# Performance work log

Measured on AMD Instinct MI355X. Metric: run time of the kernel, lower is better.

## Reference

```python
import jax, jax.numpy as jnp
import numpy as np

EMB_SIZE = 200000
DIM = 256
WALK_LEN = 80
WINDOW = 5
BATCH = 32
NEGATIVE = 5
NEG_WEIGHT = 1.0
LR = 0.025
LAP_NORM = 0.01


def _pos_index():
    # replicates init_emb2pos_index: for each center i, u-index = context j, v-index = center i
    us, vs = [], []
    for i in range(WALK_LEN):
        for j in range(max(0, i - WINDOW), i):
            us.append(j); vs.append(i)
        for j in range(i + 1, min(WALK_LEN, i + 1 + WINDOW)):
            us.append(j); vs.append(i)
    us = np.asarray(us, np.int32)
    vs = np.asarray(vs, np.int32)
    off = (np.arange(BATCH, dtype=np.int32) * WALK_LEN)[:, None]
    return (us[None, :] + off).reshape(-1), (vs[None, :] + off).reshape(-1)


def _neg_index(pos_v):
    # replicates init_emb2neg_index: u-index = center repeated NEGATIVE times per positive pair;
    # v-index = shuffled node positions from the whole batch (in-batch negatives)
    negu = np.repeat(pos_v, NEGATIVE)
    negv = np.tile(np.arange(BATCH * WALK_LEN, dtype=np.int32), NEGATIVE * WINDOW * 2)
    rng = np.random.default_rng(0)
    rng.shuffle(negv)
    return negu, negv[: len(negu)]


def setup_inputs() -> dict:
    key = jax.random.key(0)
    k1, k2, k3 = jax.random.split(key, 3)
    initrange = 1.0 / DIM
    u_weight = jax.random.uniform(k1, (EMB_SIZE, DIM), jnp.float32, -initrange, initrange)
    # original inits v to zero; use small noise so scores/grads are non-degenerate for testing
    v_weight = 0.01 * jax.random.normal(k2, (EMB_SIZE, DIM), jnp.float32)
    # sigmoid lookup table: torch.sigmoid(torch.arange(-6.01, 6.01, 0.01)) -> 1202 entries
    table = jax.nn.sigmoid(jnp.arange(1202, dtype=jnp.float32) * 0.01 - 6.01)
    table = table.at[0].set(0.0).at[-1].set(1.0)
    nodes = jax.random.randint(k3, (BATCH, WALK_LEN), 0, EMB_SIZE, dtype=jnp.int32)
    pu, pv = _pos_index()
    nu, nv = _neg_index(pv)
    return {
        "nodes": nodes,
        "u_weight": u_weight,
        "v_weight": v_weight,
        "lookup_table": table,
        "idx_posu": jnp.asarray(pu),
        "idx_posv": jnp.asarray(pv),
        "idx_negu": jnp.asarray(nu),
        "idx_negv": jnp.asarray(nv),
    }


def reference(nodes, u_weight, v_weight, lookup_table, idx_posu, idx_posv, idx_negu, idx_negv):
    flat = nodes.reshape(-1)                       # [B*L]
    emb_u = u_weight[flat]                         # [B*L, D]
    emb_v = v_weight[flat]                         # [B*L, D]

    def fast_sigmoid(s):
        idx = jnp.floor((s + 6.01) / 0.01).astype(jnp.int32)
        return lookup_table[idx]

    # positive pairs
    epu = emb_u[idx_posu]                          # [P, D]
    epv = emb_v[idx_posv]
    pos = jnp.clip(jnp.sum(epu * epv, axis=1), -6.0, 6.0)
    s = (1.0 - fast_sigmoid(pos))[:, None]
    gu_pos = s * epv + LAP_NORM * (epv - epu)
    gv_pos = s * epu + LAP_NORM * (epu - epv)
    grad_u = jnp.zeros_like(emb_u).at[idx_posu].add(gu_pos)
    grad_v = jnp.zeros_like(emb_v).at[idx_posv].add(gv_pos)

    # in-batch negative pairs
    enu = emb_u[idx_negu]                          # [P*neg, D]
    env = emb_v[idx_negv]
    neg = jnp.clip(jnp.sum(enu * env, axis=1), -6.0, 6.0)
    ns = (-fast_sigmoid(neg))[:, None]
    grad_u = grad_u.at[idx_negu].add(NEG_WEIGHT * ns * env)
    grad_v = grad_v.at[idx_negv].add(NEG_WEIGHT * ns * enu)

    # fused SGD scatter-update of the embedding tables
    new_u = u_weight.at[flat].add(LR * grad_u)
    new_v = v_weight.at[flat].add(LR * grad_v)
    return jnp.concatenate([new_u, new_v], axis=0)  # [2*EMB_SIZE, D]
```

## Files before the change

### kernel.cpp

```cpp
#include <hip/hip_runtime.h>

#define EMB      200000
#define DIM      256
#define WALK     80
#define WIN      5
#define BATCH    32
#define PPW      770
#define NPOSN    (BATCH * PPW)
#define NNEG     (NPOSN * 5)
#define NPOSIT   (BATCH * WALK)
#define LR       0.025f
#define LAP      0.01f
#define INV_STRIDE 64

#define T4          (EMB * DIM / 4)
#define CHUNK_F4    2048
#define COPY_CHUNKS (2 * T4 / CHUNK_F4)

#define INV_BLOCKS  482
#define OWN_BLOCKS  10
#define GRAD_BLOCKS 1280

typedef __attribute__((ext_vector_type(4))) int v4i;
typedef __attribute__((ext_vector_type(4))) float v4f;

__device__ __forceinline__ int Sfun(int i) {
    if (i <= 5)  return 5 * i + (i * (i - 1)) / 2;
    if (i <= 75) return 35 + 10 * (i - 5);
    return 735 + (i - 75) * 84 - ((i + 74) * (i - 75)) / 2;
}

__device__ __forceinline__ float wave_sum(float s) {
#pragma unroll
    for (int off = 32; off > 0; off >>= 1) s += __shfl_xor(s, off, 64);
    return s;
}

__device__ __forceinline__ float fast_sig(const float* __restrict__ t, float d) {
    float s = fminf(fmaxf(d, -6.0f), 6.0f);
    int idx = (int)floorf((s + 6.01f) / 0.01f);
    return t[idx];
}

__global__ void __launch_bounds__(256) k_stage(
        const int* __restrict__ nodes,
        const float* __restrict__ uw,
        const float* __restrict__ vw,
        float* __restrict__ eu,
        float* __restrict__ ev,
        v4f* __restrict__ accz,
        v4i* __restrict__ markz,
        int* __restrict__ cnt) {
    int p = blockIdx.x;
    int d = threadIdx.x;
    int node = nodes[p];
    eu[p * DIM + d] = uw[(size_t)node * DIM + d];
    ev[p * DIM + d] = vw[(size_t)node * DIM + d];
    int tid = p * 256 + d;
    if (tid < (2 * NPOSIT * DIM) / 4) accz[tid] = (v4f){0.f, 0.f, 0.f, 0.f};
    if (tid < EMB / 4) markz[tid] = (v4i){0x7FFFFFFF, 0x7FFFFFFF, 0x7FFFFFFF, 0x7FFFFFFF};
    if (d == 0) cnt[p] = 0;
}

__global__ void k_index(const int* __restrict__ negv,
                        const int* __restrict__ nodes,
                        int* __restrict__ cnt,
                        int* __restrict__ inv,
                        int* __restrict__ mark) {
    int bid = blockIdx.x;
    if (bid < INV_BLOCKS) {
        int m = bid * 256 + threadIdx.x;
        if (m < NNEG) {
            int p = negv[m];
            int slot = atomicAdd(&cnt[p], 1);
            inv[p * INV_STRIDE + slot] = m;
        }
    } else {
        int p = (bid - INV_BLOCKS) * 256 + threadIdx.x;
        if (p < NPOSIT) atomicMin(&mark[nodes[p]], p);
    }
}

__global__ void __launch_bounds__(256) k_grad(
        const int*   __restrict__ nodes,
        const float* __restrict__ table,
        const int*   __restrict__ negu,
        const int*   __restrict__ negv,
        const float* __restrict__ eu,
        const float* __restrict__ ev,
        const int*   __restrict__ cnt,
        const int*   __restrict__ inv,
        const int*   __restrict__ mark,
        float*       __restrict__ accu,
        float*       __restrict__ accv) {
    int wid  = blockIdx.x * 4 + (threadIdx.x >> 6);
    int lane = threadIdx.x & 63;
    int side = wid >= NPOSIT;
    int p    = side ? wid - NPOSIT : wid;
    int b    = p / WALK;
    int i    = p - b * WALK;
    int col  = lane * 4;

    int jlo = (i - WIN < 0) ? 0 : i - WIN;
    int jhi = (i + WIN > WALK - 1) ? WALK - 1 : i + WIN;
    int own = mark[nodes[p]];

    if (!side) {
        const float4 mu = *(const float4*)&eu[p * DIM + col];
        float gx = 0.f, gy = 0.f, gz = 0.f, gw = 0.f;

        for (int j = jlo; j <= jhi; ++j) {
            if (j == i) continue;
            int q = b * WALK + j;
            float4 qv = *(const float4*)&ev[q * DIM + col];
            float d1 = wave_sum(mu.x * qv.x + mu.y * qv.y + mu.z * qv.z + mu.w * qv.w);
            float s1 = 1.0f - fast_sig(table, d1);
            gx += s1 * qv.x + LAP * (qv.x - mu.x);
            gy += s1 * qv.y + LAP * (qv.y - mu.y);
            gz += s1 * qv.z + LAP * (qv.z - mu.z);
            gw += s1 * qv.w + LAP * (qv.w - mu.w);
        }

        int Si = Sfun(i);
        int ci = Sfun(i + 1) - Si;
        int mstart = 5 * (PPW * b + Si);
        int mcnt   = 5 * ci;
        for (int t = 0; t < mcnt; ++t) {
            int z = negv[mstart + t];
            float4 zv = *(const float4*)&ev[z * DIM + col];
            float d  = wave_sum(mu.x * zv.x + mu.y * zv.y + mu.z * zv.z + mu.w * zv.w);
            float ns = -fast_sig(table, d);
            gx += ns * zv.x; gy += ns * zv.y; gz += ns * zv.z; gw += ns * zv.w;
        }

        float* dst = &accu[(size_t)own * DIM + col];
        atomicAdd(dst + 0, gx);
        atomicAdd(dst + 1, gy);
        atomicAdd(dst + 2, gz);
        atomicAdd(dst + 3, gw);
    } else {
        const float4 mv = *(const float4*)&ev[p * DIM + col];
        float gx = 0.f, gy = 0.f, gz = 0.f, gw = 0.f;

        for (int j = jlo; j <= jhi; ++j) {
            if (j == i) continue;
            int q = b * WALK + j;
            float4 qu = *(const float4*)&eu[q * DIM + col];
            float d2 = wave_sum(qu.x * mv.x + qu.y * mv.y + qu.z * mv.z + qu.w * mv.w);
            float s2 = 1.0f - fast_sig(table, d2);
            gx += s2 * qu.x + LAP * (qu.x - mv.x);
            gy += s2 * qu.y + LAP * (qu.y - mv.y);
            gz += s2 * qu.z + LAP * (qu.z - mv.z);
            gw += s2 * qu.w + LAP * (qu.w - mv.w);
        }

        int ninv = cnt[p];
        for (int t = 0; t < ninv; ++t) {
            int m = inv[p * INV_STRIDE + t];
            int a = negu[m];
            float4 au = *(const float4*)&eu[a * DIM + col];
            float d  = wave_sum(au.x * mv.x + au.y * mv.y + au.z * mv.z + au.w * mv.w);
            float ns = -fast_sig(table, d);
            gx += ns * au.x; gy += ns * au.y; gz += ns * au.z; gw += ns * au.w;
        }

        float* dst = &accv[(size_t)own * DIM + col];
        atomicAdd(dst + 0, gx);
        atomicAdd(dst + 1, gy);
        atomicAdd(dst + 2, gz);
        atomicAdd(dst + 3, gw);
    }
}

__global__ void __launch_bounds__(256) k_copyapply(
        const float* __restrict__ uw,
        const float* __restrict__ vw,
        const float* __restrict__ accu,
        const float* __restrict__ accv,
        const int*   __restrict__ mark,
        float*       __restrict__ out) {
    size_t base = (size_t)blockIdx.x * CHUNK_F4;
    int tbl = base >= (size_t)T4;
    const float4* __restrict__ src = tbl ? (const float4*)vw : (const float4*)uw;
    const float4* __restrict__ acc = tbl ? (const float4*)accv : (const float4*)accu;
    size_t soff = tbl ? base - T4 : base;
    float4* __restrict__ dst = (float4*)out + base;
    int t = threadIdx.x;
    int c = t & 63;
#pragma unroll
    for (int k = 0; k < CHUNK_F4 / 256; ++k) {
        size_t i = soff + t + k * 256;
        int row = (int)(i >> 6);
        float4 v = src[i];
        int p = mark[row];
        if (p < NPOSIT) {
            float4 a = acc[(size_t)p * 64 + c];
            v.x += LR * a.x; v.y += LR * a.y;
            v.z += LR * a.z; v.w += LR * a.w;
        }
        dst[t + k * 256] = v;
    }
}

extern "C" void kernel_launch(void* const* d_in, const int* in_sizes, int n_in,
                              void* d_out, int out_size, void* d_ws, size_t ws_size,
                              hipStream_t stream) {
    const int*   nodes = (const int*)d_in[0];
    const float* uw    = (const float*)d_in[1];
    const float* vw    = (const float*)d_in[2];
    const float* table = (const float*)d_in[3];
    const int*   negu  = (const int*)d_in[6];
    const int*   negv  = (const int*)d_in[7];
    float* out = (float*)d_out;

    float* eu    = (float*)d_ws;
    float* ev    = eu + (size_t)NPOSIT * DIM;
    float* accu  = ev + (size_t)NPOSIT * DIM;
    float* accv  = accu + (size_t)NPOSIT * DIM;
    int*   cnt   = (int*)(accv + (size_t)NPOSIT * DIM);
    int*   inv   = cnt + NPOSIT;
    int*   mark  = inv + (size_t)NPOSIT * INV_STRIDE;

    k_stage<<<NPOSIT, DIM, 0, stream>>>(nodes, uw, vw, eu, ev,
                                        (v4f*)accu, (v4i*)mark, cnt);
    k_index<<<INV_BLOCKS + OWN_BLOCKS, 256, 0, stream>>>(negv, nodes, cnt, inv, mark);
    k_grad<<<GRAD_BLOCKS, 256, 0, stream>>>(nodes, table, negu, negv, eu, ev,
                                            cnt, inv, mark, accu, accv);
    k_copyapply<<<COPY_CHUNKS, 256, 0, stream>>>(uw, vw, accu, accv, mark, out);
}
```

Measured before the change: 243.5 us.

## Overlap bulk table copy with gradient compute and patch touched rows afterwards

The full-table copy of both embedding tables now runs as extra blocks inside the gradient kernel, so the large memory-bound copy overlaps with the gradient computation. The per-element mark lookup and accumulator read are removed from the copy. A small follow-up kernel rewrites only the rows touched by the batch, using the first position of each node, adding the scaled gradient. This removes the dependency of the copy on gradient completion, at the cost of writing touched rows twice and one more launch.

```diff
diff --git a/kernel.cpp b/kernel.cpp
--- a/kernel.cpp
+++ b/kernel.cpp
@@ -81,8 +81,10 @@
     }
 }
 
-__global__ void __launch_bounds__(256) k_grad(
+__global__ void __launch_bounds__(256) k_fused(
         const int*   __restrict__ nodes,
+        const float* __restrict__ uw,
+        const float* __restrict__ vw,
         const float* __restrict__ table,
         const int*   __restrict__ negu,
         const int*   __restrict__ negv,
@@ -92,7 +94,21 @@
         const int*   __restrict__ inv,
         const int*   __restrict__ mark,
         float*       __restrict__ accu,
-        float*       __restrict__ accv) {
+        float*       __restrict__ accv,
+        float*       __restrict__ out) {
+    if (blockIdx.x >= GRAD_BLOCKS) {
+        size_t base = (size_t)(blockIdx.x - GRAD_BLOCKS) * CHUNK_F4;
+        int tbl = base >= (size_t)T4;
+        const float4* __restrict__ src = tbl ? (const float4*)vw : (const float4*)uw;
+        size_t soff = tbl ? base - T4 : base;
+        float4* __restrict__ dst = (float4*)out + base;
+        int t = threadIdx.x;
+#pragma unroll
+        for (int k = 0; k < CHUNK_F4 / 256; ++k)
+            dst[t + k * 256] = src[soff + t + k * 256];
+        return;
+    }
+
     int wid  = blockIdx.x * 4 + (threadIdx.x >> 6);
     int lane = threadIdx.x & 63;
     int side = wid >= NPOSIT;
@@ -172,34 +188,20 @@
     }
 }
 
-__global__ void __launch_bounds__(256) k_copyapply(
-        const float* __restrict__ uw,
-        const float* __restrict__ vw,
-        const float* __restrict__ accu,
-        const float* __restrict__ accv,
-        const int*   __restrict__ mark,
-        float*       __restrict__ out) {
-    size_t base = (size_t)blockIdx.x * CHUNK_F4;
-    int tbl = base >= (size_t)T4;
-    const float4* __restrict__ src = tbl ? (const float4*)vw : (const float4*)uw;
-    const float4* __restrict__ acc = tbl ? (const float4*)accv : (const float4*)accu;
-    size_t soff = tbl ? base - T4 : base;
-    float4* __restrict__ dst = (float4*)out + base;
-    int t = threadIdx.x;
-    int c = t & 63;
-#pragma unroll
-    for (int k = 0; k < CHUNK_F4 / 256; ++k) {
-        size_t i = soff + t + k * 256;
-        int row = (int)(i >> 6);
-        float4 v = src[i];
-        int p = mark[row];
-        if (p < NPOSIT) {
-            float4 a = acc[(size_t)p * 64 + c];
-            v.x += LR * a.x; v.y += LR * a.y;
-            v.z += LR * a.z; v.w += LR * a.w;
-        }
-        dst[t + k * 256] = v;
-    }
+__global__ void k_fix(const int* __restrict__ nodes,
+                      const float* __restrict__ uw,
+                      const float* __restrict__ vw,
+                      const float* __restrict__ accu,
+                      const float* __restrict__ accv,
+                      const int* __restrict__ mark,
+                      float* __restrict__ out) {
+    int p = blockIdx.x;
+    int n = nodes[p];
+    if (mark[n] != p) return;
+    int d = threadIdx.x;
+    size_t off = (size_t)n * DIM + d;
+    out[off] = uw[off] + LR * accu[(size_t)p * DIM + d];
+    out[(size_t)EMB * DIM + off] = vw[off] + LR * accv[(size_t)p * DIM + d];
 }
 
 extern "C" void kernel_launch(void* const* d_in, const int* in_sizes, int n_in,
@@ -224,7 +226,8 @@
     k_stage<<<NPOSIT, DIM, 0, stream>>>(nodes, uw, vw, eu, ev,
                                         (v4f*)accu, (v4i*)mark, cnt);
     k_index<<<INV_BLOCKS + OWN_BLOCKS, 256, 0, stream>>>(negv, nodes, cnt, inv, mark);
-    k_grad<<<GRAD_BLOCKS, 256, 0, stream>>>(nodes, table, negu, negv, eu, ev,
-                                            cnt, inv, mark, accu, accv);
-    k_copyapply<<<COPY_CHUNKS, 256, 0, stream>>>(uw, vw, accu, accv, mark, out);
-}
+    k_fused<<<GRAD_BLOCKS + COPY_CHUNKS, 256, 0, stream>>>(
+        nodes, uw, vw, table, negu, negv, eu, ev, cnt, inv, mark,
+        accu, accv, out);
+    k_fix<<<NPOSIT, DIM, 0, stream>>>(nodes, uw, vw, accu, accv, mark, out);
+}
```

Measured after the change: 221.1 us (median of 2 runs). 1.1x faster.
